# Kernel tuning notes

Hardware: AMD Instinct MI355X
Metric: run time of the kernel (lower is better)

## Reference

```python
import jax, jax.numpy as jnp
import numpy as np

B, N, DIM, H, DH, PDIM, ED = 2, 384, 256, 4, 64, 128, 16
EPS = 1e-8


def _ln(x, g, b):
    m = x.mean(-1, keepdims=True)
    v = ((x - m) ** 2).mean(-1, keepdims=True)
    return (x - m) / jnp.sqrt(v + 1e-5) * g + b


def setup_inputs() -> dict:
    key = jax.random.key(0)
    ks = iter(jax.random.split(key, 48))
    def rn(shape, s=0.02):
        return jax.random.normal(next(ks), shape, jnp.float32) * s
    z = lambda *s: jnp.zeros(s, jnp.float32)
    o = lambda *s: jnp.ones(s, jnp.float32)
    return dict(
        feats=jax.random.normal(next(ks), (B, N, DIM), jnp.float32),
        coors=jax.random.normal(next(ks), (B, N, 3), jnp.float32),
        edges=jax.random.normal(next(ks), (B, N, N, ED), jnp.float32),
        gamma=o(DIM),
        w_qkv=rn((DIM, 3 * H * DH)),
        w_gate=z(DIM, 2 * H), b_gate=jnp.full((2 * H,), 10.0, jnp.float32),
        w_th=rn((H, H), 0.3),
        w_e1=rn((H + ED, 2 * (H + ED))), w_e2=rn((2 * (H + ED), H)),
        w_c=rn((H, H)),
        w_cg=rn((H, H)), b_cg=z(H),
        coors_scale=o(1),
        coors_combine=jax.random.normal(next(ks), (H,), jnp.float32),
        pb_w0=rn((1, PDIM)), pb_b0=z(PDIM), pb_g0=o(PDIM), pb_be0=z(PDIM),
        pb_w1=rn((PDIM, PDIM)), pb_b1=z(PDIM), pb_g1=o(PDIM), pb_be1=z(PDIM),
        pb_w2=rn((PDIM, PDIM)), pb_b2=z(PDIM), pb_g2=o(PDIM), pb_be2=z(PDIM),
        w_qkpos=rn((PDIM, H)), b_qkpos=z(H),
        w_vpos=rn((PDIM, H * DH)), b_vpos=z(H * DH),
        w_out=rn((H * DH, DIM)), b_out=z(DIM),
    )


def reference(feats, coors, edges, gamma, w_qkv, w_gate, b_gate, w_th, w_e1, w_e2,
              w_c, w_cg, b_cg, coors_scale, coors_combine,
              pb_w0, pb_b0, pb_g0, pb_be0, pb_w1, pb_b1, pb_g1, pb_be1,
              pb_w2, pb_b2, pb_g2, pb_be2, w_qkpos, b_qkpos, w_vpos, b_vpos,
              w_out, b_out):
    b, n, _ = feats.shape
    h, dh = H, DH
    x = _ln(feats, gamma, 0.0)                                  # pre-norm (beta is a zero buffer)
    rel_coors = coors[:, :, None, :] - coors[:, None, :, :]      # b i j 3
    rel_dist = jnp.linalg.norm(rel_coors, axis=-1)               # b i j

    qkv = x @ w_qkv
    q, k, v = jnp.split(qkv, 3, axis=-1)
    q = q.reshape(b, n, h, dh).transpose(0, 2, 1, 3)             # b h n d
    k = k.reshape(b, n, h, dh).transpose(0, 2, 1, 3)
    v = v.reshape(b, n, h, dh).transpose(0, 2, 1, 3)

    gates = jax.nn.sigmoid(x @ w_gate + b_gate).reshape(b, n, 2, h)
    out_gate = gates[:, :, 0].transpose(0, 2, 1)[..., None]      # b h n 1
    rel_out_gate = gates[:, :, 1].transpose(0, 2, 1)[..., None]  # b h n 1

    # dynamic position bias MLP on pairwise distances (input_dim=1)
    p = rel_dist[..., None]                                      # b i j 1
    p = jax.nn.silu(_ln(p @ pb_w0 + pb_b0, pb_g0, pb_be0))
    p = jax.nn.silu(_ln(p @ pb_w1 + pb_b1, pb_g1, pb_be1))
    p = jax.nn.silu(_ln(p @ pb_w2 + pb_b2, pb_g2, pb_be2))       # b i j pdim
    qk_pos = (p @ w_qkpos + b_qkpos).transpose(0, 3, 1, 2)       # b h i j
    value_pos = (p @ w_vpos + b_vpos).reshape(b, n, n, h, dh).transpose(0, 3, 1, 2, 4)  # b h i j d

    q = q * (dh ** -0.5)
    qk = jnp.einsum('bhid,bhjd->bhij', q, k) + qk_pos            # b h i j

    # edge MLP fused with per-head scores
    qk_e = jnp.concatenate([qk.transpose(0, 2, 3, 1), edges], axis=-1)  # b i j (h+ed)
    cmi = jax.nn.gelu(qk_e @ w_e1, approximate=False) @ w_e2     # b i j h
    qk = cmi.transpose(0, 3, 1, 2)                               # b h i j

    # coordinate attention branch (edge variant: GELU -> Linear(h,h))
    coor_weights = jax.nn.gelu(cmi, approximate=False) @ w_c     # b i j h
    coor_attn = jax.nn.softmax(coor_weights, axis=-2)            # softmax over j
    rel_sign = cmi @ w_cg + b_cg                                 # b i j h

    nrm = jnp.linalg.norm(rel_coors, axis=-1, keepdims=True)
    rel_norm = rel_coors / jnp.maximum(nrm, EPS) * coors_scale   # CoorsNorm, b i j 3

    attn = jax.nn.softmax(qk, axis=-1)
    attn = jnp.einsum('hg,bgij->bhij', w_th, attn)               # talking heads 1x1 conv

    node_out = jnp.einsum('bhij,bhjd->bhid', attn, v) \
             + jnp.einsum('bhij,bhijd->bhid', attn, value_pos)   # b h i d

    w = coor_attn * rel_sign                                     # b i j h
    coors_out = jnp.einsum('bijh,bijc->bhic', w, rel_norm)       # b h i 3

    node_out = node_out * out_gate
    coors_out = coors_out * rel_out_gate
    coors_out = jnp.einsum('bhic,h->bic', coors_out, coors_combine)
    node_out = node_out.transpose(0, 2, 1, 3).reshape(b, n, h * dh)
    return node_out @ w_out + b_out, coors_out
```

## Files before the change

### kernel.cpp

```cpp
#include <hip/hip_runtime.h>
#include <hip/hip_bf16.h>

#define B_   2
#define N_   384
#define DIM_ 256
#define H_   4
#define DH_  64
#define PD_  128
#define ED_  16
#define NU2_ ((B_ * N_ * N_) / 16)

typedef _Float16 v8h __attribute__((ext_vector_type(8)));
typedef float    v4f __attribute__((ext_vector_type(4)));

__device__ __forceinline__ float rcp_(float x) { return __builtin_amdgcn_rcpf(x); }

__device__ __forceinline__ float erf_fast(float x) {
    float ax = fabsf(x);
    float t = rcp_(fmaf(0.3275911f, ax, 1.0f));
    float y = t * fmaf(t, fmaf(t, fmaf(t, fmaf(t, 1.061405429f, -1.453152027f),
                                       1.421413741f), -0.284496736f), 0.254829592f);
    float r = 1.0f - y * __expf(-ax * ax);
    return (x < 0.f) ? -r : r;
}
__device__ __forceinline__ float gelu_(float x) {
    return 0.5f * x * (1.0f + erf_fast(x * 0.70710678118654752f));
}
__device__ __forceinline__ float silu_(float x) {
    return x * rcp_(1.0f + __expf(-x));
}

__device__ __forceinline__ float2 block_reduce256_f2(float2 v, float2* red) {
    #pragma unroll
    for (int o = 32; o > 0; o >>= 1) {
        v.x += __shfl_xor(v.x, o); v.y += __shfl_xor(v.y, o);
    }
    __syncthreads();
    if ((threadIdx.x & 63) == 0) red[threadIdx.x >> 6] = v;
    __syncthreads();
    float2 r = red[0];
    #pragma unroll
    for (int w2 = 1; w2 < 4; w2++) {
        float2 o = red[w2];
        r.x += o.x; r.y += o.y;
    }
    return r;
}

__device__ __forceinline__ void block_reduce8(float4& va, float4& vb, bool ismax,
                                              float4* red, int base) {
    #pragma unroll
    for (int o = 32; o > 0; o >>= 1) {
        float ax = __shfl_xor(va.x, o), ay = __shfl_xor(va.y, o);
        float az = __shfl_xor(va.z, o), aw = __shfl_xor(va.w, o);
        float bx = __shfl_xor(vb.x, o), by = __shfl_xor(vb.y, o);
        float bz = __shfl_xor(vb.z, o), bw = __shfl_xor(vb.w, o);
        if (ismax) {
            va.x = fmaxf(va.x, ax); va.y = fmaxf(va.y, ay); va.z = fmaxf(va.z, az); va.w = fmaxf(va.w, aw);
            vb.x = fmaxf(vb.x, bx); vb.y = fmaxf(vb.y, by); vb.z = fmaxf(vb.z, bz); vb.w = fmaxf(vb.w, bw);
        } else {
            va.x += ax; va.y += ay; va.z += az; va.w += aw;
            vb.x += bx; vb.y += by; vb.z += bz; vb.w += bw;
        }
    }
    if ((threadIdx.x & 63) == 0) {
        red[base * 8 + (threadIdx.x >> 6)]       = va;
        red[(base + 1) * 8 + (threadIdx.x >> 6)] = vb;
    }
    __syncthreads();
    va = red[base * 8]; vb = red[(base + 1) * 8];
    #pragma unroll
    for (int w2 = 1; w2 < 6; w2++) {
        float4 oa = red[base * 8 + w2], ob = red[(base + 1) * 8 + w2];
        if (ismax) {
            va.x = fmaxf(va.x, oa.x); va.y = fmaxf(va.y, oa.y); va.z = fmaxf(va.z, oa.z); va.w = fmaxf(va.w, oa.w);
            vb.x = fmaxf(vb.x, ob.x); vb.y = fmaxf(vb.y, ob.y); vb.z = fmaxf(vb.z, ob.z); vb.w = fmaxf(vb.w, ob.w);
        } else {
            va.x += oa.x; va.y += oa.y; va.z += oa.z; va.w += oa.w;
            vb.x += ob.x; vb.y += ob.y; vb.z += ob.z; vb.w += ob.w;
        }
    }
}

__global__ __launch_bounds__(256) void eq_k1(
    const float* __restrict__ feats, const float* __restrict__ gamma,
    const float* __restrict__ w_qkv, const float* __restrict__ w_gate,
    const float* __restrict__ b_gate,
    _Float16* __restrict__ qh, _Float16* __restrict__ kh, float* __restrict__ v,
    float* __restrict__ og, float* __restrict__ rg) {
    const int r0 = blockIdx.x * 2;
    const int b = r0 / N_;
    const int t = threadIdx.x;
    __shared__ float xs[2][DIM_];
    __shared__ float2 red2k[4];
    __shared__ float gredS[16][17];
    float2 f;
    f.x = feats[(long)(r0 + 0) * DIM_ + t];
    f.y = feats[(long)(r0 + 1) * DIM_ + t];
    float2 s = block_reduce256_f2(f, red2k);
    float mx = s.x * (1.f/DIM_), my = s.y * (1.f/DIM_);
    float2 d = make_float2(f.x - mx, f.y - my);
    float2 vr = block_reduce256_f2(make_float2(d.x*d.x, d.y*d.y), red2k);
    float g = gamma[t];
    xs[0][t] = d.x * rsqrtf(vr.x * (1.f/DIM_) + 1e-5f) * g;
    xs[1][t] = d.y * rsqrtf(vr.y * (1.f/DIM_) + 1e-5f) * g;
    __syncthreads();
    float acc[6];
    #pragma unroll
    for (int k = 0; k < 6; k++) acc[k] = 0.f;
    for (int c = 0; c < DIM_; c++) {
        const float* wr = w_qkv + (long)c * 768;
        float w0 = wr[t], w1 = wr[t + 256], w2 = wr[t + 512];
        #pragma unroll
        for (int r = 0; r < 2; r++) {
            float xc = xs[r][c];
            acc[r * 3 + 0] += xc * w0;
            acc[r * 3 + 1] += xc * w1;
            acc[r * 3 + 2] += xc * w2;
        }
    }
    int h = t >> 6, dd = t & 63;
    #pragma unroll
    for (int r = 0; r < 2; r++) {
        int n = r0 + r - b * N_;
        long idx = ((long)(b * H_ + h) * N_ + n) * DH_ + dd;
        qh[idx] = (_Float16)(acc[r * 3 + 0] * 0.125f);
        kh[idx] = (_Float16)(acc[r * 3 + 1]);
        v[idx]  = acc[r * 3 + 2];
    }
    {
        const int o = t & 15, chunk = t >> 4;
        const int gg = o & 7, rr = o >> 3;
        float part = 0.f;
        #pragma unroll
        for (int k = 0; k < 16; k++) {
            int c = chunk * 16 + k;
            part += xs[rr][c] * w_gate[c * 8 + gg];
        }
        gredS[chunk][o] = part;
    }
    __syncthreads();
    if (t < 16) {
        float a = b_gate[t & 7];
        #pragma unroll
        for (int k = 0; k < 16; k++) a += gredS[k][t];
        float gv = rcp_(1.0f + __expf(-a));
        int rr2 = t >> 3, g2 = t & 7;
        int n = r0 + rr2 - b * N_;
        if (g2 < 4) og[(b * H_ + g2) * N_ + n] = gv;
        else        rg[(b * H_ + (g2 - 4)) * N_ + n] = gv;
    }
}

#define MFMA16(a, b, c) __builtin_amdgcn_mfma_f32_16x16x32_f16(a, b, c, 0, 0, 0)

#define LNAPPLY(gr_, ber_)                                                        \
{                                                                                  \
    _Pragma("unroll")                                                              \
    for (int rg2 = 0; rg2 < 4; rg2++) {                                            \
        float s = 0.f, sq = 0.f;                                                   \
        _Pragma("unroll")                                                          \
        for (int nt = 0; nt < 8; nt++) {                                           \
            float v0 = acc[nt][rg2]; s += v0; sq += v0 * v0;                       \
        }                                                                          \
        s += __shfl_xor(s, 1); sq += __shfl_xor(sq, 1);                            \
        s += __shfl_xor(s, 2); sq += __shfl_xor(sq, 2);                            \
        s += __shfl_xor(s, 4); sq += __shfl_xor(sq, 4);                            \
        s += __shfl_xor(s, 8); sq += __shfl_xor(sq, 8);                            \
        float mean = s * (1.f / 128.f);                                            \
        float inv = rsqrtf(sq * (1.f / 128.f) - mean * mean + 1e-5f);              \
        int row2 = quad * 4 + rg2;                                                 \
        _Pragma("unroll")                                                          \
        for (int nt = 0; nt < 8; nt++) {                                           \
            float y = (acc[nt][rg2] - mean) * inv * gr_[nt] + ber_[nt];            \
            myslice[row2 * 136 + nt * 16 + l15] = (_Float16)silu_(y);              \
        }                                                                          \
    }                                                                              \
}

__global__ __launch_bounds__(512) __attribute__((amdgpu_waves_per_eu(2, 2)))
void eq_k2(
    const float* __restrict__ coors,
    const float* __restrict__ w0, const float* __restrict__ b0,
    const float* __restrict__ g0, const float* __restrict__ be0,
    const float* __restrict__ W1g, const float* __restrict__ b1,
    const float* __restrict__ g1, const float* __restrict__ be1,
    const float* __restrict__ W2g, const float* __restrict__ b2,
    const float* __restrict__ g2, const float* __restrict__ be2,
    const float* __restrict__ wqk, const float* __restrict__ bqk,
    const _Float16* __restrict__ qh, const _Float16* __restrict__ kh,
    _Float16* __restrict__ pT, float* __restrict__ qkpos,
    float* __restrict__ qkq) {

    extern __shared__ char smem[];
    _Float16* W1T    = (_Float16*)smem;
    _Float16* W2T    = (_Float16*)(smem + 34816);
    _Float16* slices = (_Float16*)(smem + 69632);
    _Float16* wqT    = (_Float16*)(smem + 104448);
    float*    PQR    = (float*)(smem + 108800);

    const int t = threadIdx.x;
    const int lane = t & 63, wv = t >> 6;
    const int l15 = lane & 15, quad = lane >> 4;
    _Float16* myslice = slices + wv * (16 * 136);

    for (int idx = t; idx < 16384; idx += 512) {
        int k = idx >> 7, n = idx & 127;
        W1T[n * 136 + k] = (_Float16)W1g[idx];
        W2T[n * 136 + k] = (_Float16)W2g[idx];
    }
    for (int idx = t; idx < 2048; idx += 512) {
        int n = idx >> 7, k = idx & 127;
        wqT[n * 136 + k] = (n < 4) ? (_Float16)wqk[k * 4 + n] : (_Float16)0.f;
    }
    float Sw = 0, Sb = 0, Sww = 0, Swb = 0, Sbb = 0;
    for (int c = 0; c < 128; c++) {
        float w = w0[c], bb2v = b0[c];
        Sw += w; Sb += bb2v; Sww += w * w; Swb += w * bb2v; Sbb += bb2v * bb2v;
    }
    const float mw = Sw * (1.f / 128.f), mbb = Sb * (1.f / 128.f);
    const float A2 = Sww * (1.f / 128.f) - mw * mw;
    const float AD = Swb * (1.f / 128.f) - mw * mbb;
    const float D2 = Sbb * (1.f / 128.f) - mbb * mbb;
    if (t < 128) {
        PQR[t]       = (w0[t] - mw) * g0[t];
        PQR[128 + t] = (b0[t] - mbb) * g0[t];
        PQR[256 + t] = be0[t];
    }
    float b1r[8], b2r[8], g1r[8], be1r[8], g2r[8], be2r[8];
    #pragma unroll
    for (int nt = 0; nt < 8; nt++) {
        int c = nt * 16 + l15;
        b1r[nt] = b1[c]; b2r[nt] = b2[c];
        g1r[nt] = g1[c]; be1r[nt] = be1[c];
        g2r[nt] = g2[c]; be2r[nt] = be2[c];
    }
    const float bqv = (l15 < 4) ? bqk[l15] : 0.f;
    __syncthreads();

    for (int unit = blockIdx.x * 8 + wv; unit < NU2_; unit += 256 * 8) {
        const int P0w = unit * 16;
        const int b = P0w / (N_ * N_);
        const int rem = P0w - b * (N_ * N_);
        const int ii = rem / N_;
        const int j0 = rem - ii * N_;
        const long bi = (long)(b * N_ + ii);
        const float cix = coors[(b * N_ + ii) * 3 + 0];
        const float ciy = coors[(b * N_ + ii) * 3 + 1];
        const float ciz = coors[(b * N_ + ii) * 3 + 2];
        float tt, uu;
        {
            int j = j0 + l15;
            float dx = cix - coors[(b * N_ + j) * 3 + 0];
            float dy = ciy - coors[(b * N_ + j) * 3 + 1];
            float dz = ciz - coors[(b * N_ + j) * 3 + 2];
            float d = sqrtf(dx * dx + dy * dy + dz * dz);
            float var = (d * d) * A2 + 2.f * d * AD + D2;
            float inv = rsqrtf(var + 1e-5f);
            tt = d * inv; uu = inv;
        }
        v8h A[4];
        #pragma unroll
        for (int kt = 0; kt < 4; kt++) {
            int base = kt * 32 + quad * 8;
            float4 Pa = *(const float4*)&PQR[base],       Pb = *(const float4*)&PQR[base + 4];
            float4 Qa = *(const float4*)&PQR[128 + base], Qb = *(const float4*)&PQR[128 + base + 4];
            float4 Ra = *(const float4*)&PQR[256 + base], Rb = *(const float4*)&PQR[256 + base + 4];
            float Pj[8] = {Pa.x, Pa.y, Pa.z, Pa.w, Pb.x, Pb.y, Pb.z, Pb.w};
            float Qj[8] = {Qa.x, Qa.y, Qa.z, Qa.w, Qb.x, Qb.y, Qb.z, Qb.w};
            float Rj[8] = {Ra.x, Ra.y, Ra.z, Ra.w, Rb.x, Rb.y, Rb.z, Rb.w};
            v8h av;
            #pragma unroll
            for (int jj = 0; jj < 8; jj++) {
                float y = tt * Pj[jj] + uu * Qj[jj] + Rj[jj];
                av[jj] = (_Float16)silu_(y);
            }
            A[kt] = av;
        }
        v4f acc[8];
        #pragma unroll
        for (int nt = 0; nt < 8; nt++) {
            v4f ci = {b1r[nt], b1r[nt], b1r[nt], b1r[nt]};
            acc[nt] = ci;
        }
        #pragma unroll
        for (int kt = 0; kt < 4; kt++) {
            #pragma unroll
            for (int nt = 0; nt < 8; nt++) {
                v8h Bv = *(const v8h*)&W1T[(nt * 16 + l15) * 136 + kt * 32 + quad * 8];
                acc[nt] = MFMA16(A[kt], Bv, acc[nt]);
            }
        }
        LNAPPLY(g1r, be1r)
        #pragma unroll
        for (int kt = 0; kt < 4; kt++)
            A[kt] = *(const v8h*)&myslice[l15 * 136 + kt * 32 + quad * 8];
        #pragma unroll
        for (int nt = 0; nt < 8; nt++) {
            v4f ci = {b2r[nt], b2r[nt], b2r[nt], b2r[nt]};
            acc[nt] = ci;
        }
        #pragma unroll
        for (int kt = 0; kt < 4; kt++) {
            #pragma unroll
            for (int nt = 0; nt < 8; nt++) {
                v8h Bv = *(const v8h*)&W2T[(nt * 16 + l15) * 136 + kt * 32 + quad * 8];
                acc[nt] = MFMA16(A[kt], Bv, acc[nt]);
            }
        }
        LNAPPLY(g2r, be2r)
        {
            _Float16* chunk = pT + (((long)bi * 24 + (j0 >> 4)) << 11);
            #pragma unroll
            for (int cc = 0; cc < 2; cc++) {
                int c = lane + cc * 64;
                v8h lo, hi;
                #pragma unroll
                for (int k = 0; k < 8; k++) {
                    lo[k] = myslice[k * 136 + c];
                    hi[k] = myslice[(k + 8) * 136 + c];
                }
                *(v8h*)(chunk + c * 16)     = lo;
                *(v8h*)(chunk + c * 16 + 8) = hi;
            }
        }
        {
            v4f c = {0.f, 0.f, 0.f, 0.f};
            #pragma unroll
            for (int kt = 0; kt < 4; kt++) {
                v8h av = *(const v8h*)&myslice[l15 * 136 + kt * 32 + quad * 8];
                v8h wq = *(const v8h*)&wqT[l15 * 136 + kt * 32 + quad * 8];
                c = MFMA16(av, wq, c);
            }
            if (l15 < 4) {
                #pragma unroll
                for (int rg2 = 0; rg2 < 4; rg2++) {
                    int row = quad * 4 + rg2;
                    qkpos[(long)(P0w + row) * 4 + l15] = c[rg2] + bqv;
                }
            }
        }
    }

    {
        int gw = blockIdx.x * 8 + wv;
        if (gw < 384) {
            const int bh = gw / 48;
            const int rest = gw - bh * 48;
            const int it = rest >> 1, nh = rest & 1;
            const int bb = bh >> 2, hh = bh & 3;
            const int i0 = it * 16;
            v8h A0 = *(const v8h*)&qh[((long)(bh * N_) + i0 + l15) * DH_ + quad * 8];
            v8h A1 = *(const v8h*)&qh[((long)(bh * N_) + i0 + l15) * DH_ + 32 + quad * 8];
            #pragma unroll 1
            for (int nt = 0; nt < 12; nt++) {
                int jq0 = nh * 192 + nt * 16;
                v8h B0 = *(const v8h*)&kh[((long)(bh * N_) + jq0 + l15) * DH_ + quad * 8];
                v8h B1 = *(const v8h*)&kh[((long)(bh * N_) + jq0 + l15) * DH_ + 32 + quad * 8];
                v4f c = {0.f, 0.f, 0.f, 0.f};
                c = MFMA16(A0, B0, c);
                c = MFMA16(A1, B1, c);
                #pragma unroll
                for (int rg2 = 0; rg2 < 4; rg2++) {
                    int i = i0 + quad * 4 + rg2;
                    int j = jq0 + l15;
                    long idx = (((long)(bb * N_ + i)) * N_ + j) * 4 + hh;
                    qkq[idx] = c[rg2];
                }
            }
        }
    }
}

__global__ __launch_bounds__(384) void eq_k3m(
    const float* __restrict__ edges, const float* __restrict__ qkpos,
    const float* __restrict__ qkq,
    const _Float16* __restrict__ pT, const float* __restrict__ v,
    const float* __restrict__ coors,
    const float* __restrict__ w_e1, const float* __restrict__ w_e2,
    const float* __restrict__ w_c, const float* __restrict__ w_cg,
    const float* __restrict__ b_cg, const float* __restrict__ w_th,
    const float* __restrict__ cscale, const float* __restrict__ ccomb,
    const float* __restrict__ og, const float* __restrict__ rg,
    const float* __restrict__ w_vpos, const float* __restrict__ b_vpos,
    const float* __restrict__ w_out, const float* __restrict__ b_out,
    float* __restrict__ out0, float* __restrict__ out1) {
    int row = blockIdx.x;
    int b = row / N_, i = row - b * N_;
    int j = threadIdx.x;
    __shared__ _Float16 we1h[20 * 40];
    __shared__ float we2[40 * 4];
    __shared__ float wcs[16], wcgs[16], bcgs[4], wths[16];
    __shared__ float attnS[4 * N_];
    __shared__ float apS[2 * 4 * PD_];
    __shared__ float nodeS[256];
    __shared__ float4 red4[50];

    for (int idx = j; idx < 800; idx += 384) we1h[idx] = (_Float16)w_e1[idx];
    if (j < 160) we2[j] = w_e2[j];
    if (j < 16) { wcs[j] = w_c[j]; wcgs[j] = w_cg[j]; wths[j] = w_th[j]; }
    if (j < 4) bcgs[j] = b_cg[j];
    __syncthreads();

    long pair = ((long)row) * N_ + j;
    float in20[20];
    {
        float4 qp = *(const float4*)(qkpos + pair * 4);
        float4 qq = *(const float4*)(qkq + pair * 4);
        in20[0] = qp.x + qq.x; in20[1] = qp.y + qq.y;
        in20[2] = qp.z + qq.z; in20[3] = qp.w + qq.w;
    }
    const float4* ep = (const float4*)(edges + pair * ED_);
    float4 e0 = ep[0], e1 = ep[1], e2 = ep[2], e3 = ep[3];
    in20[4] = e0.x;  in20[5] = e0.y;  in20[6] = e0.z;  in20[7] = e0.w;
    in20[8] = e1.x;  in20[9] = e1.y;  in20[10] = e1.z; in20[11] = e1.w;
    in20[12] = e2.x; in20[13] = e2.y; in20[14] = e2.z; in20[15] = e2.w;
    in20[16] = e3.x; in20[17] = e3.y; in20[18] = e3.z; in20[19] = e3.w;

    float c0 = 0, c1 = 0, c2 = 0, c3 = 0;
    #pragma unroll 1
    for (int oc = 0; oc < 5; oc++) {
        float a8[8] = {0.f, 0.f, 0.f, 0.f, 0.f, 0.f, 0.f, 0.f};
        #pragma unroll
        for (int c = 0; c < 20; c++) {
            float xc = in20[c];
            v8h wv = *(const v8h*)&we1h[c * 40 + oc * 8];
            #pragma unroll
            for (int o2 = 0; o2 < 8; o2++) a8[o2] += xc * (float)wv[o2];
        }
        #pragma unroll
        for (int o = 0; o < 8; o++) {
            float gg = gelu_(a8[o]);
            float4 w2v = *(const float4*)&we2[(oc * 8 + o) * 4];
            c0 += gg * w2v.x; c1 += gg * w2v.y; c2 += gg * w2v.z; c3 += gg * w2v.w;
        }
    }
    float cmi[4] = {c0, c1, c2, c3};
    float gc[4], cp[4], rs[4];
    #pragma unroll
    for (int h = 0; h < 4; h++) gc[h] = gelu_(cmi[h]);
    #pragma unroll
    for (int h = 0; h < 4; h++) {
        cp[h] = gc[0] * wcs[h] + gc[1] * wcs[4 + h] + gc[2] * wcs[8 + h] + gc[3] * wcs[12 + h];
        rs[h] = cmi[0] * wcgs[h] + cmi[1] * wcgs[4 + h] + cmi[2] * wcgs[8 + h] + cmi[3] * wcgs[12 + h] + bcgs[h];
    }

    float dx = coors[(b * N_ + i) * 3 + 0] - coors[(b * N_ + j) * 3 + 0];
    float dy = coors[(b * N_ + i) * 3 + 1] - coors[(b * N_ + j) * 3 + 1];
    float dz = coors[(b * N_ + i) * 3 + 2] - coors[(b * N_ + j) * 3 + 2];
    float nrm = sqrtf(dx * dx + dy * dy + dz * dz);
    float sc = cscale[0] * rcp_(fmaxf(nrm, 1e-8f));
    float rx = dx * sc, ry = dy * sc, rz = dz * sc;

    float4 m4  = make_float4(cmi[0], cmi[1], cmi[2], cmi[3]);
    float4 cm4 = make_float4(cp[0], cp[1], cp[2], cp[3]);
    block_reduce8(m4, cm4, true, red4, 0);
    float e[4], ec[4];
    e[0] = __expf(cmi[0] - m4.x); e[1] = __expf(cmi[1] - m4.y);
    e[2] = __expf(cmi[2] - m4.z); e[3] = __expf(cmi[3] - m4.w);
    ec[0] = __expf(cp[0] - cm4.x); ec[1] = __expf(cp[1] - cm4.y);
    ec[2] = __expf(cp[2] - cm4.z); ec[3] = __expf(cp[3] - cm4.w);
    float4 l4  = make_float4(e[0], e[1], e[2], e[3]);
    float4 cl4 = make_float4(ec[0], ec[1], ec[2], ec[3]);
    block_reduce8(l4, cl4, false, red4, 2);

    float sm[4] = {e[0] * rcp_(l4.x), e[1] * rcp_(l4.y), e[2] * rcp_(l4.z), e[3] * rcp_(l4.w)};
    #pragma unroll
    for (int h = 0; h < 4; h++)
        attnS[h * N_ + j] = wths[h * 4 + 0] * sm[0] + wths[h * 4 + 1] * sm[1]
                          + wths[h * 4 + 2] * sm[2] + wths[h * 4 + 3] * sm[3];

    float w[4] = {ec[0] * rcp_(cl4.x) * rs[0], ec[1] * rcp_(cl4.y) * rs[1],
                  ec[2] * rcp_(cl4.z) * rs[2], ec[3] * rcp_(cl4.w) * rs[3]};
    float rv[12];
    #pragma unroll
    for (int h = 0; h < 4; h++) { rv[h] = w[h] * rx; rv[4 + h] = w[h] * ry; rv[8 + h] = w[h] * rz; }
    #pragma unroll
    for (int o = 32; o > 0; o >>= 1) {
        #pragma unroll
        for (int k = 0; k < 12; k++) rv[k] += __shfl_xor(rv[k], o);
    }
    if ((j & 63) == 0) {
        int wid = j >> 6;
        red4[32 + wid * 3 + 0] = make_float4(rv[0], rv[1], rv[2], rv[3]);
        red4[32 + wid * 3 + 1] = make_float4(rv[4], rv[5], rv[6], rv[7]);
        red4[32 + wid * 3 + 2] = make_float4(rv[8], rv[9], rv[10], rv[11]);
    }
    __syncthreads();
    if (j == 0) {
        float4 sx4 = red4[32], sy4 = red4[33], sz4 = red4[34];
        #pragma unroll
        for (int w2 = 1; w2 < 6; w2++) {
            float4 ax = red4[32 + w2 * 3 + 0], ay = red4[32 + w2 * 3 + 1], az = red4[32 + w2 * 3 + 2];
            sx4.x += ax.x; sx4.y += ax.y; sx4.z += ax.z; sx4.w += ax.w;
            sy4.x += ay.x; sy4.y += ay.y; sy4.z += ay.z; sy4.w += ay.w;
            sz4.x += az.x; sz4.y += az.y; sz4.z += az.z; sz4.w += az.w;
        }
        float f0 = ccomb[0] * rg[(b * H_ + 0) * N_ + i];
        float f1 = ccomb[1] * rg[(b * H_ + 1) * N_ + i];
        float f2 = ccomb[2] * rg[(b * H_ + 2) * N_ + i];
        float f3 = ccomb[3] * rg[(b * H_ + 3) * N_ + i];
        out1[(b * N_ + i) * 3 + 0] = f0 * sx4.x + f1 * sx4.y + f2 * sx4.z + f3 * sx4.w;
        out1[(b * N_ + i) * 3 + 1] = f0 * sy4.x + f1 * sy4.y + f2 * sy4.z + f3 * sy4.w;
        out1[(b * N_ + i) * 3 + 2] = f0 * sz4.x + f1 * sz4.y + f2 * sz4.z + f3 * sz4.w;
    }

    if (j < 128) {
        const int lane = j & 63, l15d = lane & 15, quadd = lane >> 4;
        const int parity = j >> 6;
        const int hh = l15d & 3;
        const float msk = (l15d < 4) ? 1.f : 0.f;
        v4f acc[8];
        #pragma unroll
        for (int nt = 0; nt < 8; nt++) { v4f z = {0.f, 0.f, 0.f, 0.f}; acc[nt] = z; }
        #pragma unroll 2
        for (int kth = 0; kth < 6; kth++) {
            int kt = parity * 6 + kth;
            float4 a0 = *(const float4*)&attnS[hh * N_ + kt * 32 + quadd * 8];
            float4 a1 = *(const float4*)&attnS[hh * N_ + kt * 32 + quadd * 8 + 4];
            v8h Af;
            Af[0] = (_Float16)(a0.x * msk); Af[1] = (_Float16)(a0.y * msk);
            Af[2] = (_Float16)(a0.z * msk); Af[3] = (_Float16)(a0.w * msk);
            Af[4] = (_Float16)(a1.x * msk); Af[5] = (_Float16)(a1.y * msk);
            Af[6] = (_Float16)(a1.z * msk); Af[7] = (_Float16)(a1.w * msk);
            const _Float16* chunkp = pT + (((long)row * 24 + kt * 2 + (quadd >> 1)) << 11)
                                        + ((quadd & 1) << 3);
            #pragma unroll
            for (int nt = 0; nt < 8; nt++) {
                v8h Bv = *(const v8h*)&chunkp[(nt * 16 + l15d) * 16];
                acc[nt] = MFMA16(Af, Bv, acc[nt]);
            }
        }
        if (quadd == 0) {
            #pragma unroll
            for (int nt = 0; nt < 8; nt++)
                #pragma unroll
                for (int rg2 = 0; rg2 < 4; rg2++)
                    apS[parity * 512 + rg2 * 128 + nt * 16 + l15d] = acc[nt][rg2];
        }
    } else {
        int tt = j - 128, h = tt >> 6, d = tt & 63;
        float acc0 = 0, acc1 = 0, acc2 = 0, acc3 = 0;
        const float* vp = v + ((long)(b * H_ + h) * N_) * DH_ + d;
        #pragma unroll 8
        for (int jj = 0; jj < N_; jj += 4) {
            float4 a = *(const float4*)&attnS[h * N_ + jj];
            acc0 += a.x * vp[(long)(jj + 0) * DH_];
            acc1 += a.y * vp[(long)(jj + 1) * DH_];
            acc2 += a.z * vp[(long)(jj + 2) * DH_];
            acc3 += a.w * vp[(long)(jj + 3) * DH_];
        }
        nodeS[tt] = (acc0 + acc1) + (acc2 + acc3);
    }
    __syncthreads();

    float nv = 0;
    if (j < 256) {
        int h = j >> 6, d = j & 63;
        float accp = 0;
        const float* wv = w_vpos + h * DH_ + d;
        #pragma unroll 4
        for (int c4 = 0; c4 < 32; c4++) {
            float4 p0 = *(const float4*)&apS[h * 128 + c4 * 4];
            float4 p1 = *(const float4*)&apS[512 + h * 128 + c4 * 4];
            accp += (p0.x + p1.x) * wv[(long)(c4 * 4 + 0) * (H_ * DH_)]
                  + (p0.y + p1.y) * wv[(long)(c4 * 4 + 1) * (H_ * DH_)]
                  + (p0.z + p1.z) * wv[(long)(c4 * 4 + 2) * (H_ * DH_)]
                  + (p0.w + p1.w) * wv[(long)(c4 * 4 + 3) * (H_ * DH_)];
        }
        float Sh = wths[h * 4 + 0] + wths[h * 4 + 1] + wths[h * 4 + 2] + wths[h * 4 + 3];
        nv = (nodeS[j] + accp + Sh * b_vpos[h * DH_ + d]) * og[(b * H_ + h) * N_ + i];
    }
    __syncthreads();
    if (j < 256) nodeS[j] = nv;
    __syncthreads();

    if (j < 256) {
        float acc = b_out[j];
        const float* wo = w_out + j;
        #pragma unroll 4
        for (int c4 = 0; c4 < 64; c4++) {
            float4 nv4 = *(const float4*)&nodeS[c4 * 4];
            acc += nv4.x * wo[(long)(c4 * 4 + 0) * 256]
                 + nv4.y * wo[(long)(c4 * 4 + 1) * 256]
                 + nv4.z * wo[(long)(c4 * 4 + 2) * 256]
                 + nv4.w * wo[(long)(c4 * 4 + 3) * 256];
        }
        out0[(long)row * 256 + j] = acc;
    }
}

extern "C" void kernel_launch(void* const* d_in, const int* in_sizes, int n_in,
                              void* d_out, int out_size, void* d_ws, size_t ws_size,
                              hipStream_t stream) {
    (void)in_sizes; (void)n_in; (void)out_size; (void)ws_size;
    const float* feats   = (const float*)d_in[0];
    const float* coors   = (const float*)d_in[1];
    const float* edges   = (const float*)d_in[2];
    const float* gamma   = (const float*)d_in[3];
    const float* w_qkv   = (const float*)d_in[4];
    const float* w_gate  = (const float*)d_in[5];
    const float* b_gate  = (const float*)d_in[6];
    const float* w_th    = (const float*)d_in[7];
    const float* w_e1    = (const float*)d_in[8];
    const float* w_e2    = (const float*)d_in[9];
    const float* w_c     = (const float*)d_in[10];
    const float* w_cg    = (const float*)d_in[11];
    const float* b_cg    = (const float*)d_in[12];
    const float* cscale  = (const float*)d_in[13];
    const float* ccomb   = (const float*)d_in[14];
    const float* pb_w0   = (const float*)d_in[15];
    const float* pb_b0   = (const float*)d_in[16];
    const float* pb_g0   = (const float*)d_in[17];
    const float* pb_be0  = (const float*)d_in[18];
    const float* pb_w1   = (const float*)d_in[19];
    const float* pb_b1   = (const float*)d_in[20];
    const float* pb_g1   = (const float*)d_in[21];
    const float* pb_be1  = (const float*)d_in[22];
    const float* pb_w2   = (const float*)d_in[23];
    const float* pb_b2   = (const float*)d_in[24];
    const float* pb_g2   = (const float*)d_in[25];
    const float* pb_be2  = (const float*)d_in[26];
    const float* w_qkpos = (const float*)d_in[27];
    const float* b_qkpos = (const float*)d_in[28];
    const float* w_vpos  = (const float*)d_in[29];
    const float* b_vpos  = (const float*)d_in[30];
    const float* w_out   = (const float*)d_in[31];
    const float* b_out   = (const float*)d_in[32];

    char* ws = (char*)d_ws;
    _Float16* qh   = (_Float16*)(ws + 0);
    _Float16* kh   = (_Float16*)(ws + 393216);
    float* v       = (float*)(ws + 786432);
    float* og      = (float*)(ws + 1572864);
    float* rg      = (float*)(ws + 1585152);
    float* qkpos   = (float*)(ws + 1597440);
    _Float16* pT   = (_Float16*)(ws + 6316032);
    float* qkq     = (float*)(ws + 81813504);

    float* out0 = (float*)d_out;
    float* out1 = out0 + (long)B_ * N_ * DIM_;

    const int K2_LDS = 110336;
    hipFuncSetAttribute((const void*)eq_k2, hipFuncAttributeMaxDynamicSharedMemorySize, K2_LDS);

    eq_k1<<<384, 256, 0, stream>>>(feats, gamma, w_qkv, w_gate, b_gate, qh, kh, v, og, rg);
    eq_k2<<<256, 512, K2_LDS, stream>>>(coors, pb_w0, pb_b0, pb_g0, pb_be0,
                                        pb_w1, pb_b1, pb_g1, pb_be1,
                                        pb_w2, pb_b2, pb_g2, pb_be2,
                                        w_qkpos, b_qkpos, qh, kh, pT, qkpos, qkq);
    eq_k3m<<<B_ * N_, 384, 0, stream>>>(edges, qkpos, qkq, pT, v, coors,
                                        w_e1, w_e2, w_c, w_cg, b_cg, w_th,
                                        cscale, ccomb, og, rg,
                                        w_vpos, b_vpos, w_out, b_out, out0, out1);
}
```

Baseline: 306.5 us.

## Exploit pairwise-distance symmetry to compute positional MLP only for upper-triangle tiles

Measured after the change: 296.7 us. -3.2%, faster.

```diff
diff --git a/kernel.cpp b/kernel.cpp
--- a/kernel.cpp
+++ b/kernel.cpp
@@ -8,7 +8,9 @@
 #define DH_  64
 #define PD_  128
 #define ED_  16
-#define NU2_ ((B_ * N_ * N_) / 16)
+#define NT_  24
+#define TPB_ 300
+#define JOBS_ 600
 
 typedef _Float16 v8h __attribute__((ext_vector_type(8)));
 typedef float    v4f __attribute__((ext_vector_type(4)));
@@ -195,14 +197,13 @@
     extern __shared__ char smem[];
     _Float16* W1T    = (_Float16*)smem;
     _Float16* W2T    = (_Float16*)(smem + 34816);
-    _Float16* slices = (_Float16*)(smem + 69632);
-    _Float16* wqT    = (_Float16*)(smem + 104448);
-    float*    PQR    = (float*)(smem + 108800);
+    _Float16* wqT    = (_Float16*)(smem + 69632);
+    float*    PQR    = (float*)(smem + 73984);
+    _Float16* slices = (_Float16*)(smem + 75520);
 
     const int t = threadIdx.x;
     const int lane = t & 63, wv = t >> 6;
     const int l15 = lane & 15, quad = lane >> 4;
-    _Float16* myslice = slices + wv * (16 * 136);
 
     for (int idx = t; idx < 16384; idx += 512) {
         int k = idx >> 7, n = idx & 127;
@@ -238,113 +239,146 @@
     const float bqv = (l15 < 4) ? bqk[l15] : 0.f;
     __syncthreads();
 
-    for (int unit = blockIdx.x * 8 + wv; unit < NU2_; unit += 256 * 8) {
-        const int P0w = unit * 16;
-        const int b = P0w / (N_ * N_);
-        const int rem = P0w - b * (N_ * N_);
-        const int ii = rem / N_;
-        const int j0 = rem - ii * N_;
-        const long bi = (long)(b * N_ + ii);
-        const float cix = coors[(b * N_ + ii) * 3 + 0];
-        const float ciy = coors[(b * N_ + ii) * 3 + 1];
-        const float ciz = coors[(b * N_ + ii) * 3 + 2];
-        float tt, uu;
-        {
-            int j = j0 + l15;
-            float dx = cix - coors[(b * N_ + j) * 3 + 0];
-            float dy = ciy - coors[(b * N_ + j) * 3 + 1];
-            float dz = ciz - coors[(b * N_ + j) * 3 + 2];
-            float d = sqrtf(dx * dx + dy * dy + dz * dz);
-            float var = (d * d) * A2 + 2.f * d * AD + D2;
-            float inv = rsqrtf(var + 1e-5f);
-            tt = d * inv; uu = inv;
-        }
-        v8h A[4];
-        #pragma unroll
-        for (int kt = 0; kt < 4; kt++) {
-            int base = kt * 32 + quad * 8;
-            float4 Pa = *(const float4*)&PQR[base],       Pb = *(const float4*)&PQR[base + 4];
-            float4 Qa = *(const float4*)&PQR[128 + base], Qb = *(const float4*)&PQR[128 + base + 4];
-            float4 Ra = *(const float4*)&PQR[256 + base], Rb = *(const float4*)&PQR[256 + base + 4];
-            float Pj[8] = {Pa.x, Pa.y, Pa.z, Pa.w, Pb.x, Pb.y, Pb.z, Pb.w};
-            float Qj[8] = {Qa.x, Qa.y, Qa.z, Qa.w, Qb.x, Qb.y, Qb.z, Qb.w};
-            float Rj[8] = {Ra.x, Ra.y, Ra.z, Ra.w, Rb.x, Rb.y, Rb.z, Rb.w};
-            v8h av;
-            #pragma unroll
-            for (int jj = 0; jj < 8; jj++) {
-                float y = tt * Pj[jj] + uu * Qj[jj] + Rj[jj];
-                av[jj] = (_Float16)silu_(y);
-            }
-            A[kt] = av;
-        }
-        v4f acc[8];
-        #pragma unroll
-        for (int nt = 0; nt < 8; nt++) {
-            v4f ci = {b1r[nt], b1r[nt], b1r[nt], b1r[nt]};
-            acc[nt] = ci;
-        }
-        #pragma unroll
-        for (int kt = 0; kt < 4; kt++) {
+    for (int jo = blockIdx.x; jo < JOBS_; jo += 256) {
+        int b = jo / TPB_;
+        int tt2 = jo - b * TPB_;
+        int it = 0, rl = NT_;
+        while (tt2 >= rl) { tt2 -= rl; it++; rl--; }
+        const int jt = it + tt2;
+        const int j0 = jt * 16;
+
+        #pragma unroll 1
+        for (int rr = 0; rr < 2; rr++) {
+            const int r = wv + rr * 8;
+            const int ii = it * 16 + r;
+            _Float16* myslice = slices + r * 2176;
+            const float cix = coors[(b * N_ + ii) * 3 + 0];
+            const float ciy = coors[(b * N_ + ii) * 3 + 1];
+            const float ciz = coors[(b * N_ + ii) * 3 + 2];
+            float tt, uu;
+            {
+                int j = j0 + l15;
+                float dx = cix - coors[(b * N_ + j) * 3 + 0];
+                float dy = ciy - coors[(b * N_ + j) * 3 + 1];
+                float dz = ciz - coors[(b * N_ + j) * 3 + 2];
+                float d = sqrtf(dx * dx + dy * dy + dz * dz);
+                float var = (d * d) * A2 + 2.f * d * AD + D2;
+                float inv = rsqrtf(var + 1e-5f);
+                tt = d * inv; uu = inv;
+            }
+            v8h A[4];
+            #pragma unroll
+            for (int kt = 0; kt < 4; kt++) {
+                int base = kt * 32 + quad * 8;
+                float4 Pa = *(const float4*)&PQR[base],       Pb = *(const float4*)&PQR[base + 4];
+                float4 Qa = *(const float4*)&PQR[128 + base], Qb = *(const float4*)&PQR[128 + base + 4];
+                float4 Ra = *(const float4*)&PQR[256 + base], Rb = *(const float4*)&PQR[256 + base + 4];
+                float Pj[8] = {Pa.x, Pa.y, Pa.z, Pa.w, Pb.x, Pb.y, Pb.z, Pb.w};
+                float Qj[8] = {Qa.x, Qa.y, Qa.z, Qa.w, Qb.x, Qb.y, Qb.z, Qb.w};
+                float Rj[8] = {Ra.x, Ra.y, Ra.z, Ra.w, Rb.x, Rb.y, Rb.z, Rb.w};
+                v8h av;
+                #pragma unroll
+                for (int jj = 0; jj < 8; jj++) {
+                    float y = tt * Pj[jj] + uu * Qj[jj] + Rj[jj];
+                    av[jj] = (_Float16)silu_(y);
+                }
+                A[kt] = av;
+            }
+            v4f acc[8];
             #pragma unroll
             for (int nt = 0; nt < 8; nt++) {
-                v8h Bv = *(const v8h*)&W1T[(nt * 16 + l15) * 136 + kt * 32 + quad * 8];
-                acc[nt] = MFMA16(A[kt], Bv, acc[nt]);
-            }
-        }
-        LNAPPLY(g1r, be1r)
-        #pragma unroll
-        for (int kt = 0; kt < 4; kt++)
-            A[kt] = *(const v8h*)&myslice[l15 * 136 + kt * 32 + quad * 8];
-        #pragma unroll
-        for (int nt = 0; nt < 8; nt++) {
-            v4f ci = {b2r[nt], b2r[nt], b2r[nt], b2r[nt]};
-            acc[nt] = ci;
-        }
-        #pragma unroll
-        for (int kt = 0; kt < 4; kt++) {
+                v4f ci = {b1r[nt], b1r[nt], b1r[nt], b1r[nt]};
+                acc[nt] = ci;
+            }
+            #pragma unroll
+            for (int kt = 0; kt < 4; kt++) {
+                #pragma unroll
+                for (int nt = 0; nt < 8; nt++) {
+                    v8h Bv = *(const v8h*)&W1T[(nt * 16 + l15) * 136 + kt * 32 + quad * 8];
+                    acc[nt] = MFMA16(A[kt], Bv, acc[nt]);
+                }
+            }
+            LNAPPLY(g1r, be1r)
+            #pragma unroll
+            for (int kt = 0; kt < 4; kt++)
+                A[kt] = *(const v8h*)&myslice[l15 * 136 + kt * 32 + quad * 8];
             #pragma unroll
             for (int nt = 0; nt < 8; nt++) {
-                v8h Bv = *(const v8h*)&W2T[(nt * 16 + l15) * 136 + kt * 32 + quad * 8];
-                acc[nt] = MFMA16(A[kt], Bv, acc[nt]);
-            }
-        }
-        LNAPPLY(g2r, be2r)
-        {
-            _Float16* chunk = pT + (((long)bi * 24 + (j0 >> 4)) << 11);
-            #pragma unroll
-            for (int cc = 0; cc < 2; cc++) {
-                int c = lane + cc * 64;
-                v8h lo, hi;
-                #pragma unroll
-                for (int k = 0; k < 8; k++) {
-                    lo[k] = myslice[k * 136 + c];
-                    hi[k] = myslice[(k + 8) * 136 + c];
-                }
-                *(v8h*)(chunk + c * 16)     = lo;
-                *(v8h*)(chunk + c * 16 + 8) = hi;
-            }
-        }
-        {
-            v4f c = {0.f, 0.f, 0.f, 0.f};
+                v4f ci = {b2r[nt], b2r[nt], b2r[nt], b2r[nt]};
+                acc[nt] = ci;
+            }
             #pragma unroll
             for (int kt = 0; kt < 4; kt++) {
-                v8h av = *(const v8h*)&myslice[l15 * 136 + kt * 32 + quad * 8];
-                v8h wq = *(const v8h*)&wqT[l15 * 136 + kt * 32 + quad * 8];
-                c = MFMA16(av, wq, c);
-            }
-            if (l15 < 4) {
-                #pragma unroll
-                for (int rg2 = 0; rg2 < 4; rg2++) {
-                    int row = quad * 4 + rg2;
-                    qkpos[(long)(P0w + row) * 4 + l15] = c[rg2] + bqv;
-                }
-            }
-        }
+                #pragma unroll
+                for (int nt = 0; nt < 8; nt++) {
+                    v8h Bv = *(const v8h*)&W2T[(nt * 16 + l15) * 136 + kt * 32 + quad * 8];
+                    acc[nt] = MFMA16(A[kt], Bv, acc[nt]);
+                }
+            }
+            LNAPPLY(g2r, be2r)
+            {
+                v4f c = {0.f, 0.f, 0.f, 0.f};
+                #pragma unroll
+                for (int kt = 0; kt < 4; kt++) {
+                    v8h av = *(const v8h*)&myslice[l15 * 136 + kt * 32 + quad * 8];
+                    v8h wq = *(const v8h*)&wqT[l15 * 136 + kt * 32 + quad * 8];
+                    c = MFMA16(av, wq, c);
+                }
+                if (l15 < 4) {
+                    #pragma unroll
+                    for (int rg2 = 0; rg2 < 4; rg2++) {
+                        int rowj = quad * 4 + rg2;
+                        float val = c[rg2] + bqv;
+                        qkpos[((long)(b * N_ + ii) * N_ + j0 + rowj) * 4 + l15] = val;
+                        if (it != jt)
+                            qkpos[((long)(b * N_ + j0 + rowj) * N_ + ii) * 4 + l15] = val;
+                    }
+                }
+            }
+        }
+        __syncthreads();
+
+        #pragma unroll
+        for (int rx = 0; rx < 2; rx++) {
+            const int r2 = wv * 2 + rx;
+            {
+                const _Float16* src = slices + r2 * 2176;
+                _Float16* chunk = pT + (((long)(b * N_ + it * 16 + r2) * 24 + jt) << 11);
+                #pragma unroll
+                for (int cc = 0; cc < 2; cc++) {
+                    int c = lane + cc * 64;
+                    v8h lo, hi;
+                    #pragma unroll
+                    for (int k = 0; k < 8; k++) {
+                        lo[k] = src[k * 136 + c];
+                        hi[k] = src[(k + 8) * 136 + c];
+                    }
+                    *(v8h*)(chunk + c * 16)     = lo;
+                    *(v8h*)(chunk + c * 16 + 8) = hi;
+                }
+            }
+            if (it != jt) {
+                _Float16* chunk = pT + (((long)(b * N_ + jt * 16 + r2) * 24 + it) << 11);
+                #pragma unroll
+                for (int cc = 0; cc < 2; cc++) {
+                    int c = lane + cc * 64;
+                    v8h lo, hi;
+                    #pragma unroll
+                    for (int r = 0; r < 8; r++) {
+                        lo[r] = slices[r * 2176 + r2 * 136 + c];
+                        hi[r] = slices[(r + 8) * 2176 + r2 * 136 + c];
+                    }
+                    *(v8h*)(chunk + c * 16)     = lo;
+                    *(v8h*)(chunk + c * 16 + 8) = hi;
+                }
+            }
+        }
+        __syncthreads();
     }
 
     {
-        int gw = blockIdx.x * 8 + wv;
-        if (gw < 384) {
+        int gw = (blockIdx.x - 88) * 8 + wv;
+        if (blockIdx.x >= 88 && gw < 384) {
             const int bh = gw / 48;
             const int rest = gw - bh * 48;
             const int it = rest >> 1, nh = rest & 1;
@@ -641,7 +675,7 @@
     float* out0 = (float*)d_out;
     float* out1 = out0 + (long)B_ * N_ * DIM_;
 
-    const int K2_LDS = 110336;
+    const int K2_LDS = 145152;
     hipFuncSetAttribute((const void*)eq_k2, hipFuncAttributeMaxDynamicSharedMemorySize, K2_LDS);
 
     eq_k1<<<384, 256, 0, stream>>>(feats, gamma, w_qkv, w_gate, b_gate, qh, kh, v, og, rg);
```
